# Kernel optimization log

Hardware: AMD Instinct MI355X
Metric: run time of the kernel (lower is better)

The kernel has to match this reference:

```python
import jax, jax.numpy as jnp
import numpy as np

D_MODEL = 1024
NUM_HEADS = 16
HEAD_DIM = D_MODEL // NUM_HEADS
THETA = 10000.0
BATCH, SEQ = 2, 2048


def rope(x, token_positions):
    # x: [b, h, s, d]; token_positions: [s]
    d = x.shape[-1]
    freqs = 1.0 / THETA ** (jnp.arange(0, d, 2, dtype=jnp.float32)[: d // 2] / d)
    ang = token_positions.astype(jnp.float32)[:, None] * freqs[None, :]  # [s, d/2]
    cos, sin = jnp.cos(ang), jnp.sin(ang)
    xr = x.reshape(*x.shape[:-1], d // 2, 2)
    x_even, x_odd = xr[..., 0], xr[..., 1]
    out_even = x_even * cos - x_odd * sin
    out_odd = x_even * sin + x_odd * cos
    return jnp.stack([out_even, out_odd], axis=-1).reshape(x.shape)


def setup_inputs() -> dict:
    key = jax.random.key(0)
    ks = jax.random.split(key, 5)
    std = np.sqrt(2.0 / (D_MODEL + D_MODEL))
    mk = lambda k: (jax.random.truncated_normal(k, -3.0, 3.0, (D_MODEL, D_MODEL), jnp.float32) * std)
    return {
        "x": jax.random.normal(ks[0], (BATCH, SEQ, D_MODEL), jnp.float32),
        "Wq": mk(ks[1]),
        "Wk": mk(ks[2]),
        "Wv": mk(ks[3]),
        "Wo": mk(ks[4]),
        "casual_mask": jnp.tril(jnp.ones((SEQ, SEQ), dtype=bool)),
        "token_positions": jnp.arange(SEQ, dtype=jnp.int32),
    }


def reference(x, Wq, Wk, Wv, Wo, casual_mask, token_positions):
    b, s, _ = x.shape
    split = lambda t: t.reshape(b, s, NUM_HEADS, HEAD_DIM).transpose(0, 2, 1, 3)
    q = split(x @ Wq.T)  # [b, h, s, d]
    k = split(x @ Wk.T)
    v = split(x @ Wv.T)
    q = rope(q, token_positions)
    k = rope(k, token_positions)
    scores = jnp.einsum("bhqd,bhkd->bhqk", q, k) / np.sqrt(HEAD_DIM)
    scores = jnp.where(casual_mask, scores, -jnp.inf)
    probs = jax.nn.softmax(scores, axis=-1)
    out = jnp.einsum("bhqk,bhkd->bhqd", probs, v)
    out = out.transpose(0, 2, 1, 3).reshape(b, s, D_MODEL)
    return out @ Wo.T
```

## Files before the change

### kernel.cpp

```cpp
#include <hip/hip_runtime.h>
#include <hip/hip_bf16.h>

#define SEQ_LEN 2048
#define NBATCH 2
#define DM 1024
#define NH 16
#define HD 64
#define NR (NBATCH * SEQ_LEN)
#define NQKV (3 * DM)

typedef __attribute__((ext_vector_type(8))) short bf16x8;
typedef __attribute__((ext_vector_type(4))) float f32x4;

__device__ __forceinline__ short f2b(float f) {
    __hip_bfloat16 h = __float2bfloat16(f);
    return *reinterpret_cast<short*>(&h);
}
__device__ __forceinline__ float b2f(short s) {
    union { unsigned u; float f; } x;
    x.u = ((unsigned)(unsigned short)s) << 16;
    return x.f;
}

__device__ __forceinline__ void gload_lds16(const void* g, void* l) {
    __builtin_amdgcn_global_load_lds(
        (const __attribute__((address_space(1))) unsigned int*)g,
        (__attribute__((address_space(3))) unsigned int*)l, 16, 0, 0);
}

__global__ __launch_bounds__(256) void cvt_all(
    const float* __restrict__ x,  const float* __restrict__ wq,
    const float* __restrict__ wk, const float* __restrict__ wv,
    const float* __restrict__ wo,
    __hip_bfloat16* __restrict__ xb, __hip_bfloat16* __restrict__ wqkvb,
    __hip_bfloat16* __restrict__ wob) {
    int id = blockIdx.x;
    const float* src; __hip_bfloat16* dst;
    if (id < 4096) { src = x + (size_t)id * 1024; dst = xb + (size_t)id * 1024; }
    else {
        int k = id - 4096, seg = k >> 10;
        size_t off = (size_t)(k & 1023) * 1024;
        if      (seg == 0) { src = wq + off; dst = wqkvb + off; }
        else if (seg == 1) { src = wk + off; dst = wqkvb + (1u << 20) + off; }
        else if (seg == 2) { src = wv + off; dst = wqkvb + (2u << 20) + off; }
        else               { src = wo + off; dst = wob + off; }
    }
    int i = threadIdx.x * 4;
    float4 v = *(const float4*)(src + i);
    dst[i + 0] = __float2bfloat16(v.x);
    dst[i + 1] = __float2bfloat16(v.y);
    dst[i + 2] = __float2bfloat16(v.z);
    dst[i + 3] = __float2bfloat16(v.w);
}

__device__ __forceinline__ void store_c(float* p, float v) { *p = v; }
__device__ __forceinline__ void store_c(__hip_bfloat16* p, float v) {
    *p = __float2bfloat16(v);
}

template <typename CT>
__global__ __launch_bounds__(256) void gemm128(
    const __hip_bfloat16* __restrict__ A,
    const __hip_bfloat16* __restrict__ B,
    CT* __restrict__ C, int K, int ldc) {
    __shared__ __hip_bfloat16 As[128 * 32];
    __shared__ __hip_bfloat16 Bs[128 * 32];
    const int t    = threadIdx.x;
    const int wave = t >> 6;
    const int lane = t & 63;
    const int quad = lane >> 4;
    const int l16  = lane & 15;
    const int wy = wave >> 1, wx = wave & 1;
    const int m0 = blockIdx.x * 128, n0 = blockIdx.y * 128;

    const int r0 = wave * 32 + (lane >> 2);
    const int c0 = (lane & 3) * 8;
    const __hip_bfloat16* Ag0 = A + (size_t)(m0 + r0) * K + c0;
    const __hip_bfloat16* Ag1 = Ag0 + (size_t)16 * K;
    const __hip_bfloat16* Bg0 = B + (size_t)(n0 + r0) * K + c0;
    const __hip_bfloat16* Bg1 = Bg0 + (size_t)16 * K;
    __hip_bfloat16* lA0 = &As[r0 * 32 + c0];
    __hip_bfloat16* lA1 = &As[(r0 + 16) * 32 + c0];
    __hip_bfloat16* lB0 = &Bs[r0 * 32 + c0];
    __hip_bfloat16* lB1 = &Bs[(r0 + 16) * 32 + c0];

    f32x4 acc[4][4];
#pragma unroll
    for (int i = 0; i < 4; i++)
#pragma unroll
        for (int j = 0; j < 4; j++) acc[i][j] = (f32x4){0.f, 0.f, 0.f, 0.f};

    for (int k0 = 0; k0 < K; k0 += 32) {
        __syncthreads();
        gload_lds16(Ag0 + k0, lA0);
        gload_lds16(Ag1 + k0, lA1);
        gload_lds16(Bg0 + k0, lB0);
        gload_lds16(Bg1 + k0, lB1);
        __syncthreads();

        bf16x8 af[4], bfr[4];
#pragma unroll
        for (int rb = 0; rb < 4; rb++)
            af[rb] = *(const bf16x8*)&As[(wy * 64 + rb * 16 + l16) * 32 + quad * 8];
#pragma unroll
        for (int cb = 0; cb < 4; cb++)
            bfr[cb] = *(const bf16x8*)&Bs[(wx * 64 + cb * 16 + l16) * 32 + quad * 8];
#pragma unroll
        for (int rb = 0; rb < 4; rb++)
#pragma unroll
            for (int cb = 0; cb < 4; cb++)
                acc[rb][cb] = __builtin_amdgcn_mfma_f32_16x16x32_bf16(
                    af[rb], bfr[cb], acc[rb][cb], 0, 0, 0);
    }

#pragma unroll
    for (int rb = 0; rb < 4; rb++)
#pragma unroll
        for (int r = 0; r < 4; r++) {
            size_t ro = (size_t)(m0 + wy * 64 + rb * 16 + quad * 4 + r) * ldc;
#pragma unroll
            for (int cb = 0; cb < 4; cb++)
                store_c(&C[ro + n0 + wx * 64 + cb * 16 + l16], acc[rb][cb][r]);
        }
}

__global__ __launch_bounds__(256) void rope_kernel(
    __hip_bfloat16* __restrict__ QKV, const int* __restrict__ pos) {
    int idx = blockIdx.x * 256 + threadIdx.x;
    int row  = idx >> 8;
    int tcol = idx & 255;
    int col0 = tcol * 8;
    int head = col0 >> 6;
    int i0   = (col0 & 63) >> 1;
    float p  = (float)pos[row & (SEQ_LEN - 1)];
    float scale = (head < NH) ? 0.125f : 1.0f;
    __hip_bfloat16* ptr = QKV + (size_t)row * NQKV + col0;
    bf16x8 v = *(const bf16x8*)ptr;
    bf16x8 o;
#pragma unroll
    for (int k = 0; k < 4; k++) {
        float fr = __expf(-(float)(2 * (i0 + k)) * (9.210340371976184f / 64.0f));
        float ang = p * fr;
        float sn = sinf(ang), cs = cosf(ang);
        float e  = b2f(v[2 * k]);
        float od = b2f(v[2 * k + 1]);
        o[2 * k]     = f2b((e * cs - od * sn) * scale);
        o[2 * k + 1] = f2b((e * sn + od * cs) * scale);
    }
    *(bf16x8*)ptr = o;
}

__global__ __launch_bounds__(256) void transpose_v_kernel(
    const __hip_bfloat16* __restrict__ QKV, __hip_bfloat16* __restrict__ Vtg) {
    __shared__ short Ts[64][72];
    const int t  = threadIdx.x;
    const int r0 = blockIdx.x * 64;
    const int h  = blockIdx.y;
    const int b  = r0 >> 11;
    const int sb = r0 & (SEQ_LEN - 1);

    const int lr  = t >> 3;
    const int lcq = (t & 7) * 8;
#pragma unroll
    for (int pass = 0; pass < 2; pass++) {
        int rr = lr + pass * 32;
        int pc = 4 * (rr & 15) + (rr >> 4);
        bf16x8 v = *(const bf16x8*)(QKV + (size_t)(r0 + rr) * NQKV + 2 * DM + h * HD + lcq);
#pragma unroll
        for (int e = 0; e < 8; e++) Ts[lcq + e][pc] = v[e];
    }
    __syncthreads();
    const int dr = t >> 3;
    const int sc = (t & 7) * 8;
#pragma unroll
    for (int pass = 0; pass < 2; pass++) {
        int dd = dr + pass * 32;
        bf16x8 v = *(const bf16x8*)&Ts[dd][sc];
        *(bf16x8*)(Vtg + ((size_t)(b * NH + h) * HD + dd) * SEQ_LEN + sb + sc) = v;
    }
}

__global__ __launch_bounds__(512, 2) void attn_kernel(
    const __hip_bfloat16* __restrict__ QK,
    const __hip_bfloat16* __restrict__ Vtg,
    __hip_bfloat16* __restrict__ O) {
    __shared__ short Ps[256][72];

    const int t    = threadIdx.x;
    const int wave = t >> 6;
    const int team = wave >> 2;
    const int w4   = wave & 3;
    const int lane = t & 63;
    const int quad = lane >> 4;
    const int l16  = lane & 15;
    const int pairIdx = blockIdx.x;
    const int h    = blockIdx.y;
    const int b    = blockIdx.z;

    const int qt   = team == 0 ? pairIdx : 15 - pairIdx;
    const int row0 = qt * 128 + w4 * 32;

    bf16x8 qf[2][2];
#pragma unroll
    for (int g = 0; g < 2; g++) {
        const __hip_bfloat16* qp =
            QK + (size_t)(b * SEQ_LEN + row0 + g * 16 + l16) * NQKV + h * HD + quad * 8;
        qf[g][0] = *(const bf16x8*)qp;
        qf[g][1] = *(const bf16x8*)(qp + 32);
    }

    f32x4 o[2][4];
    float l_p[2][4];
#pragma unroll
    for (int g = 0; g < 2; g++)
#pragma unroll
        for (int r = 0; r < 4; r++) {
            o[g][r] = (f32x4){0.f, 0.f, 0.f, 0.f};
            l_p[g][r] = 0.f;
        }

    const __hip_bfloat16* kbase = QK + (size_t)(b * SEQ_LEN) * NQKV + DM + h * HD;
    const __hip_bfloat16* vbase = Vtg + (size_t)((b * NH + h) * HD) * SEQ_LEN;
    const int ktmax = (row0 + 31) >> 6;

    auto load_k = [&](bf16x8 kf[4][2], int kt) {
#pragma unroll
        for (int kb = 0; kb < 4; kb++) {
            const __hip_bfloat16* kp =
                kbase + (size_t)(kt * 64 + kb * 16 + l16) * NQKV + quad * 8;
            kf[kb][0] = *(const bf16x8*)kp;
            kf[kb][1] = *(const bf16x8*)(kp + 32);
        }
    };

    auto step = [&](bf16x8 kf[4][2], int kt) {
        bf16x8 vf[4][2];
#pragma unroll
        for (int db = 0; db < 4; db++) {
            const __hip_bfloat16* vp =
                vbase + (size_t)(db * 16 + l16) * SEQ_LEN + kt * 64 + quad * 8;
            vf[db][0] = *(const bf16x8*)vp;
            vf[db][1] = *(const bf16x8*)(vp + 32);
        }

        f32x4 s[2][4];
#pragma unroll
        for (int g = 0; g < 2; g++)
#pragma unroll
            for (int kb = 0; kb < 4; kb++) {
                f32x4 z = {0.f, 0.f, 0.f, 0.f};
                z = __builtin_amdgcn_mfma_f32_16x16x32_bf16(qf[g][0], kf[kb][0], z, 0, 0, 0);
                z = __builtin_amdgcn_mfma_f32_16x16x32_bf16(qf[g][1], kf[kb][1], z, 0, 0, 0);
                s[g][kb] = z;
            }

        if (kt == ktmax) {
#pragma unroll
            for (int g = 0; g < 2; g++)
#pragma unroll
                for (int kb = 0; kb < 4; kb++) {
                    int key = kt * 64 + kb * 16 + l16;
#pragma unroll
                    for (int r = 0; r < 4; r++) {
                        int rowg = row0 + g * 16 + quad * 4 + r;
                        if (key > rowg) s[g][kb][r] = -1e30f;
                    }
                }
        }

#pragma unroll
        for (int g = 0; g < 2; g++)
#pragma unroll
            for (int r = 0; r < 4; r++) {
                float p0 = __expf(s[g][0][r]);
                float p1 = __expf(s[g][1][r]);
                float p2 = __expf(s[g][2][r]);
                float p3 = __expf(s[g][3][r]);
                l_p[g][r] += (p0 + p1) + (p2 + p3);
                int prow = wave * 32 + g * 16 + quad * 4 + r;
                short4 pk;
                pk.x = f2b(p0); pk.y = f2b(p1); pk.z = f2b(p2); pk.w = f2b(p3);
                *(short4*)&Ps[prow][4 * l16] = pk;
            }

#pragma unroll
        for (int g = 0; g < 2; g++) {
            bf16x8 pf0 = *(const bf16x8*)&Ps[wave * 32 + g * 16 + l16][quad * 8];
            bf16x8 pf1 = *(const bf16x8*)&Ps[wave * 32 + g * 16 + l16][32 + quad * 8];
#pragma unroll
            for (int db = 0; db < 4; db++) {
                o[g][db] = __builtin_amdgcn_mfma_f32_16x16x32_bf16(pf0, vf[db][0], o[g][db], 0, 0, 0);
                o[g][db] = __builtin_amdgcn_mfma_f32_16x16x32_bf16(pf1, vf[db][1], o[g][db], 0, 0, 0);
            }
        }
    };

    bf16x8 kfA[4][2], kfB[4][2];
    load_k(kfA, 0);
    int kt = 0;
    while (true) {
        if (kt < ktmax) load_k(kfB, kt + 1);
        step(kfA, kt);
        kt++;
        if (kt > ktmax) break;
        if (kt < ktmax) load_k(kfA, kt + 1);
        step(kfB, kt);
        kt++;
        if (kt > ktmax) break;
    }

#pragma unroll
    for (int g = 0; g < 2; g++)
#pragma unroll
        for (int r = 0; r < 4; r++) {
            float rs = l_p[g][r];
            rs += __shfl_xor(rs, 1);
            rs += __shfl_xor(rs, 2);
            rs += __shfl_xor(rs, 4);
            rs += __shfl_xor(rs, 8);
            float inv = 1.0f / rs;
            size_t ro = (size_t)(b * SEQ_LEN + row0 + g * 16 + quad * 4 + r) * DM + h * HD;
            O[ro +  0 + l16] = __float2bfloat16(o[g][0][r] * inv);
            O[ro + 16 + l16] = __float2bfloat16(o[g][1][r] * inv);
            O[ro + 32 + l16] = __float2bfloat16(o[g][2][r] * inv);
            O[ro + 48 + l16] = __float2bfloat16(o[g][3][r] * inv);
        }
}

extern "C" void kernel_launch(void* const* d_in, const int* in_sizes, int n_in,
                              void* d_out, int out_size, void* d_ws, size_t ws_size,
                              hipStream_t stream) {
    const float* x  = (const float*)d_in[0];
    const float* Wq = (const float*)d_in[1];
    const float* Wk = (const float*)d_in[2];
    const float* Wv = (const float*)d_in[3];
    const float* Wo = (const float*)d_in[4];
    const int* pos = (const int*)d_in[6];
    float* out = (float*)d_out;

    char* w = (char*)d_ws;
    const size_t MiB = 1024 * 1024;
    __hip_bfloat16* xb    = (__hip_bfloat16*)(w + 0 * MiB);
    __hip_bfloat16* Ab    = (__hip_bfloat16*)(w + 0 * MiB);
    __hip_bfloat16* Wqkvb = (__hip_bfloat16*)(w + 8 * MiB);
    __hip_bfloat16* Wob   = (__hip_bfloat16*)(w + 14 * MiB);
    __hip_bfloat16* QKVb  = (__hip_bfloat16*)(w + 16 * MiB);
    __hip_bfloat16* Vtg   = (__hip_bfloat16*)(w + 40 * MiB);

    cvt_all<<<8192, 256, 0, stream>>>(x, Wq, Wk, Wv, Wo, xb, Wqkvb, Wob);

    gemm128<__hip_bfloat16><<<dim3(NR / 128, NQKV / 128), 256, 0, stream>>>(
        xb, Wqkvb, QKVb, DM, NQKV);

    rope_kernel<<<NR * 2048 / 8 / 256, 256, 0, stream>>>(QKVb, pos);

    transpose_v_kernel<<<dim3(NR / 64, NH), 256, 0, stream>>>(QKVb, Vtg);

    attn_kernel<<<dim3(8, NH, NBATCH), 512, 0, stream>>>(QKVb, Vtg, Ab);

    gemm128<float><<<dim3(NR / 128, DM / 128), 256, 0, stream>>>(
        Ab, Wob, out, DM, DM);
}
```

Before: 235.0 us.

## Software-pipeline attention loop: overlap QK/exp of next tile with PV of previous

The attention inner loop is split into stages (load V, read P from LDS, QK+exp+write P, PV MMA) and reordered so the QK and exp work for tile kt runs while the PV product for tile kt-1 is issued. This aims to hide LDS and global-load latency and let MFMA and exp work interleave. The Q scale now folds in log2(e), so exp uses the native exp2 instruction instead of __expf. The cost is more live registers for the V and P fragments, which can lower occupancy.

```diff
diff --git a/kernel.cpp b/kernel.cpp
--- a/kernel.cpp
+++ b/kernel.cpp
@@ -133,7 +133,7 @@
     int head = col0 >> 6;
     int i0   = (col0 & 63) >> 1;
     float p  = (float)pos[row & (SEQ_LEN - 1)];
-    float scale = (head < NH) ? 0.125f : 1.0f;
+    float scale = (head < NH) ? 0.18033688011112042f : 1.0f;
     __hip_bfloat16* ptr = QKV + (size_t)row * NQKV + col0;
     bf16x8 v = *(const bf16x8*)ptr;
     bf16x8 o;
@@ -223,6 +223,8 @@
     const __hip_bfloat16* vbase = Vtg + (size_t)((b * NH + h) * HD) * SEQ_LEN;
     const int ktmax = (row0 + 31) >> 6;
 
+    bf16x8 kfA[4][2], kfB[4][2], vf[4][2], pf[2][2];
+
     auto load_k = [&](bf16x8 kf[4][2], int kt) {
 #pragma unroll
         for (int kb = 0; kb < 4; kb++) {
@@ -232,9 +234,7 @@
             kf[kb][1] = *(const bf16x8*)(kp + 32);
         }
     };
-
-    auto step = [&](bf16x8 kf[4][2], int kt) {
-        bf16x8 vf[4][2];
+    auto load_v = [&](int kt) {
 #pragma unroll
         for (int db = 0; db < 4; db++) {
             const __hip_bfloat16* vp =
@@ -242,7 +242,15 @@
             vf[db][0] = *(const bf16x8*)vp;
             vf[db][1] = *(const bf16x8*)(vp + 32);
         }
-
+    };
+    auto read_p = [&]() {
+#pragma unroll
+        for (int g = 0; g < 2; g++) {
+            pf[g][0] = *(const bf16x8*)&Ps[wave * 32 + g * 16 + l16][quad * 8];
+            pf[g][1] = *(const bf16x8*)&Ps[wave * 32 + g * 16 + l16][32 + quad * 8];
+        }
+    };
+    auto qk_exp_write = [&](bf16x8 kf[4][2], int kt) {
         f32x4 s[2][4];
 #pragma unroll
         for (int g = 0; g < 2; g++)
@@ -253,7 +261,6 @@
                 z = __builtin_amdgcn_mfma_f32_16x16x32_bf16(qf[g][1], kf[kb][1], z, 0, 0, 0);
                 s[g][kb] = z;
             }
-
         if (kt == ktmax) {
 #pragma unroll
             for (int g = 0; g < 2; g++)
@@ -267,47 +274,55 @@
                     }
                 }
         }
-
 #pragma unroll
         for (int g = 0; g < 2; g++)
 #pragma unroll
             for (int r = 0; r < 4; r++) {
-                float p0 = __expf(s[g][0][r]);
-                float p1 = __expf(s[g][1][r]);
-                float p2 = __expf(s[g][2][r]);
-                float p3 = __expf(s[g][3][r]);
+                float p0 = __builtin_amdgcn_exp2f(s[g][0][r]);
+                float p1 = __builtin_amdgcn_exp2f(s[g][1][r]);
+                float p2 = __builtin_amdgcn_exp2f(s[g][2][r]);
+                float p3 = __builtin_amdgcn_exp2f(s[g][3][r]);
                 l_p[g][r] += (p0 + p1) + (p2 + p3);
                 int prow = wave * 32 + g * 16 + quad * 4 + r;
                 short4 pk;
                 pk.x = f2b(p0); pk.y = f2b(p1); pk.z = f2b(p2); pk.w = f2b(p3);
                 *(short4*)&Ps[prow][4 * l16] = pk;
             }
-
-#pragma unroll
-        for (int g = 0; g < 2; g++) {
-            bf16x8 pf0 = *(const bf16x8*)&Ps[wave * 32 + g * 16 + l16][quad * 8];
-            bf16x8 pf1 = *(const bf16x8*)&Ps[wave * 32 + g * 16 + l16][32 + quad * 8];
+    };
+    auto pv = [&]() {
+#pragma unroll
+        for (int g = 0; g < 2; g++)
 #pragma unroll
             for (int db = 0; db < 4; db++) {
-                o[g][db] = __builtin_amdgcn_mfma_f32_16x16x32_bf16(pf0, vf[db][0], o[g][db], 0, 0, 0);
-                o[g][db] = __builtin_amdgcn_mfma_f32_16x16x32_bf16(pf1, vf[db][1], o[g][db], 0, 0, 0);
+                o[g][db] = __builtin_amdgcn_mfma_f32_16x16x32_bf16(pf[g][0], vf[db][0], o[g][db], 0, 0, 0);
+                o[g][db] = __builtin_amdgcn_mfma_f32_16x16x32_bf16(pf[g][1], vf[db][1], o[g][db], 0, 0, 0);
             }
-        }
-    };
-
-    bf16x8 kfA[4][2], kfB[4][2];
+    };
+
     load_k(kfA, 0);
-    int kt = 0;
-    while (true) {
-        if (kt < ktmax) load_k(kfB, kt + 1);
-        step(kfA, kt);
+    if (ktmax >= 1) load_k(kfB, 1);
+    qk_exp_write(kfA, 0);
+
+    int kt = 1;
+    while (kt <= ktmax) {
+        load_v(kt - 1);
+        read_p();
+        if (kt < ktmax) load_k(kfA, kt + 1);
+        qk_exp_write(kfB, kt);
+        pv();
         kt++;
         if (kt > ktmax) break;
-        if (kt < ktmax) load_k(kfA, kt + 1);
-        step(kfB, kt);
+        load_v(kt - 1);
+        read_p();
+        if (kt < ktmax) load_k(kfB, kt + 1);
+        qk_exp_write(kfA, kt);
+        pv();
         kt++;
-        if (kt > ktmax) break;
-    }
+    }
+
+    load_v(ktmax);
+    read_p();
+    pv();
 
 #pragma unroll
     for (int g = 0; g < 2; g++)
```

Measured after the change: 234.8 us. Within noise of the previous version (-0.1%).
